# Optimization experiments

Hardware: AMD Instinct MI355X
Metric: run time of the kernel (lower is better)

Reference implementation:

```python
import jax, jax.numpy as jnp
import numpy as np

T, B, IN, H1, H2, OUT = 1024, 512, 20, 128, 64, 3

def _uniform(key, shape, bound):
    return jax.random.uniform(key, shape, jnp.float32, -bound, bound)

def setup_inputs() -> dict:
    key = jax.random.key(0)
    ks = jax.random.split(key, 11)
    b1 = 1.0 / np.sqrt(H1)
    b2 = 1.0 / np.sqrt(H2)
    return {
        "x": jax.random.normal(ks[0], (T, B, IN), jnp.float32),
        "W_ih0": _uniform(ks[1], (4 * H1, IN), b1),
        "W_hh0": _uniform(ks[2], (4 * H1, H1), b1),
        "b_ih0": _uniform(ks[3], (4 * H1,), b1),
        "b_hh0": _uniform(ks[4], (4 * H1,), b1),
        "W_ih1": _uniform(ks[5], (4 * H2, H1), b2),
        "W_hh1": _uniform(ks[6], (4 * H2, H2), b2),
        "b_ih1": _uniform(ks[7], (4 * H2,), b2),
        "b_hh1": _uniform(ks[8], (4 * H2,), b2),
        "W_d": _uniform(ks[9], (OUT, H2), b2),
        "b_d": _uniform(ks[10], (OUT,), b2),
    }

def _lstm_layer(x, W_ih, W_hh, b_ih, b_hh, hidden):
    # x: (T, B, in_dim); PyTorch gate order: i, f, g, o
    batch = x.shape[1]
    x_proj = jnp.einsum("tbi,gi->tbg", x, W_ih) + (b_ih + b_hh)  # (T,B,4H)

    def step(carry, xp):
        h, c = carry
        gates = xp + h @ W_hh.T  # (B,4H)
        i, f, g, o = jnp.split(gates, 4, axis=-1)
        i = jax.nn.sigmoid(i)
        f = jax.nn.sigmoid(f)
        g = jnp.tanh(g)
        o = jax.nn.sigmoid(o)
        c = f * c + i * g
        h = o * jnp.tanh(c)
        return (h, c), h

    h0 = jnp.zeros((batch, hidden), x.dtype)
    c0 = jnp.zeros((batch, hidden), x.dtype)
    _, ys = jax.lax.scan(step, (h0, c0), x_proj)
    return ys  # (T, B, H)

def reference(x, W_ih0, W_hh0, b_ih0, b_hh0, W_ih1, W_hh1, b_ih1, b_hh1, W_d, b_d):
    h1 = _lstm_layer(x, W_ih0, W_hh0, b_ih0, b_hh0, H1)   # (T,B,128)
    h2 = _lstm_layer(h1, W_ih1, W_hh1, b_ih1, b_hh1, H2)  # (T,B,64)
    # Faithful to original: lstm_out[:, -1, :] in seq-first layout picks the
    # last batch element at every timestep -> (T, 64)
    last = h2[:, -1, :]
    act = jax.nn.relu(last)
    # Dropout in eval mode is identity.
    return act @ W_d.T + b_d  # (T, 3)
```

## Files before the change

### kernel.cpp

```cpp
#include <hip/hip_runtime.h>
#include <hip/hip_bf16.h>


#define T_STEPS 1024
#define BATCH   512
#define IN_F    20
#define H1_     128
#define H2_     64
#define OUT_F   3
#define G1_     (4*H1_)
#define G2_     (4*H2_)

typedef float f4 __attribute__((ext_vector_type(4)));
typedef unsigned int u32;
typedef u32 u4 __attribute__((ext_vector_type(4)));
typedef _Float16 h2t __attribute__((ext_vector_type(2)));

__device__ __forceinline__ float sigmoidf_(float x) {
    return 1.0f / (1.0f + __expf(-x));
}
__device__ __forceinline__ float tanhf_(float x) {
    return 1.0f - 2.0f / (__expf(2.0f * x) + 1.0f);
}
__device__ __forceinline__ h2t as_h2(u32 v) {
    union { u32 u; h2t h; } c; c.u = v; return c.h;
}
__device__ __forceinline__ u32 pkh(float a, float b) {
    union { _Float16 h[2]; u32 u; } c;
    c.h[0] = (_Float16)a; c.h[1] = (_Float16)b; return c.u;
}
__device__ __forceinline__ float fdot2_(h2t a, h2t b, float c) {
#if __has_builtin(__builtin_amdgcn_fdot2)
    return __builtin_amdgcn_fdot2(a, b, c, false);
#else
    float d = c;
    asm("v_dot2_f32_f16 %0, %1, %2, %0" : "+v"(d) : "v"(a), "v"(b));
    return d;
#endif
}
__device__ __forceinline__ u4 packq(const float* p) {
    const f4 a = *(const f4*)p;
    const f4 b = *(const f4*)(p + 4);
    u4 pk;
    pk.x = pkh(a.x, a.y); pk.y = pkh(a.z, a.w);
    pk.z = pkh(b.x, b.y); pk.w = pkh(b.z, b.w);
    return pk;
}

#define LO_SCALE_INV 0.000244140625f

#define DOTQ(WQ, HH, HL)                                                      \
    { const u4 hh_ = (HH); const u4 hl_ = (HL);                               \
      a0 = fdot2_(as_h2((WQ).x), as_h2(hh_.x), a0);                           \
      a1 = fdot2_(as_h2((WQ).y), as_h2(hh_.y), a1);                           \
      a0 = fdot2_(as_h2((WQ).z), as_h2(hh_.z), a0);                           \
      a1 = fdot2_(as_h2((WQ).w), as_h2(hh_.w), a1);                           \
      a2 = fdot2_(as_h2((WQ).x), as_h2(hl_.x), a2);                           \
      a3 = fdot2_(as_h2((WQ).y), as_h2(hl_.y), a3);                           \
      a2 = fdot2_(as_h2((WQ).z), as_h2(hl_.z), a2);                           \
      a3 = fdot2_(as_h2((WQ).w), as_h2(hl_.w), a3); }

__global__ void xproj_kernel(const float* __restrict__ x,
                             const float* __restrict__ W_ih0,
                             const float* __restrict__ b_ih0,
                             const float* __restrict__ b_hh0,
                             float* __restrict__ xp1)
{
    const int t = blockIdx.x;
    const int g = threadIdx.x;
    const float* xr = x + ((size_t)t * BATCH + (BATCH - 1)) * IN_F;
    const float* w  = W_ih0 + g * IN_F;
    float acc = b_ih0[g] + b_hh0[g];
#pragma unroll
    for (int i = 0; i < IN_F; ++i) acc = fmaf(xr[i], w[i], acc);
    xp1[t * G1_ + g] = acc;
}

__global__ void pack_kernel(const float* __restrict__ W_hh0,
                            const float* __restrict__ W_hh1,
                            u4* __restrict__ wpk1,
                            u4* __restrict__ wpk2)
{
    const int idx = blockIdx.x * blockDim.x + threadIdx.x;
    if (idx < 8192) {
        const int q = idx >> 10, r = idx & 1023;
        const int g = r & 511, hf = r >> 9;
        wpk1[idx] = packq(W_hh0 + (size_t)g * H1_ + hf * 64 + q * 8);
    } else if (idx < 8192 + 2048) {
        const int i2 = idx - 8192;
        const int q = i2 >> 10, r2 = i2 & 1023;
        const int g2 = r2 & 255, qf = r2 >> 8;
        wpk2[i2] = packq(W_hh1 + (size_t)g2 * H2_ + qf * 16 + q * 8);
    }
}

__global__ __attribute__((amdgpu_flat_work_group_size(1024, 1024),
                          amdgpu_waves_per_eu(4, 4)))
void lstm1_kernel(const float* __restrict__ xp1,
                  const u4* __restrict__ wpk1,
                  float* __restrict__ h1seq)
{
    const int tid = threadIdx.x;
    const int g   = tid & 511;
    const int hf  = tid >> 9;
    const int r   = hf * 512 + g;

    __shared__ u4    shhi[16];
    __shared__ u4    shlo[16];
    __shared__ float sp1[1024];

    if (tid < 16) { shhi[tid] = u4{0,0,0,0}; shlo[tid] = u4{0,0,0,0}; }
    float c1 = 0.0f;
    __syncthreads();

    const u4* wb = wpk1 + r;
    float xp_cur = (hf == 0) ? xp1[g] : 0.0f;

    for (int t = 0; t < T_STEPS; ++t) {
        float xp_next = 0.0f;
        if (hf == 0) {
            const int tn = (t + 1 < T_STEPS) ? (t + 1) : (T_STEPS - 1);
            xp_next = xp1[(size_t)tn * G1_ + g];
        }
        const u4 w0_ = wb[0 * 1024], w1_ = wb[1 * 1024];
        const u4 w2_ = wb[2 * 1024], w3_ = wb[3 * 1024];
        const u4 w4_ = wb[4 * 1024], w5_ = wb[5 * 1024];
        const u4 w6_ = wb[6 * 1024], w7_ = wb[7 * 1024];

        float a0 = 0.f, a1 = 0.f, a2 = 0.f, a3 = 0.f;
        DOTQ(w0_, shhi[hf * 8 + 0], shlo[hf * 8 + 0]);
        DOTQ(w1_, shhi[hf * 8 + 1], shlo[hf * 8 + 1]);
        DOTQ(w2_, shhi[hf * 8 + 2], shlo[hf * 8 + 2]);
        DOTQ(w3_, shhi[hf * 8 + 3], shlo[hf * 8 + 3]);
        DOTQ(w4_, shhi[hf * 8 + 4], shlo[hf * 8 + 4]);
        DOTQ(w5_, shhi[hf * 8 + 5], shlo[hf * 8 + 5]);
        DOTQ(w6_, shhi[hf * 8 + 6], shlo[hf * 8 + 6]);
        DOTQ(w7_, shhi[hf * 8 + 7], shlo[hf * 8 + 7]);

        sp1[g * 2 + hf] = ((a0 + a1) + LO_SCALE_INV * (a2 + a3)) + xp_cur;
        __syncthreads();

        if (tid < H1_) {
            const float vi = sp1[tid * 2]              + sp1[tid * 2 + 1];
            const float vf = sp1[(H1_ + tid) * 2]      + sp1[(H1_ + tid) * 2 + 1];
            const float vg = sp1[(2 * H1_ + tid) * 2]  + sp1[(2 * H1_ + tid) * 2 + 1];
            const float vo = sp1[(3 * H1_ + tid) * 2]  + sp1[(3 * H1_ + tid) * 2 + 1];
            c1 = fmaf(sigmoidf_(vf), c1, sigmoidf_(vi) * tanhf_(vg));
            const float h = sigmoidf_(vo) * tanhf_(c1);
            const _Float16 hh16 = (_Float16)h;
            const float hrem = (h - (float)hh16) * 4096.0f;
            ((_Float16*)shhi)[tid] = hh16;
            ((_Float16*)shlo)[tid] = (_Float16)hrem;
            h1seq[(size_t)t * H1_ + tid] = h;
        }
        __syncthreads();
        xp_cur = xp_next;
    }
}

__global__ void xproj2_kernel(const float* __restrict__ h1seq,
                              const float* __restrict__ W_ih1,
                              const float* __restrict__ b_ih1,
                              const float* __restrict__ b_hh1,
                              float* __restrict__ xp2)
{
    const int t = blockIdx.x;
    const int g = threadIdx.x;
    __shared__ f4 sh[H1_ / 4];
    if (g < H1_ / 4) sh[g] = ((const f4*)(h1seq + (size_t)t * H1_))[g];
    __syncthreads();
    const f4* w = (const f4*)(W_ih1 + (size_t)g * H1_);
    float ax = 0.f, ay = 0.f, az = 0.f, aw = 0.f;
#pragma unroll
    for (int k = 0; k < H1_ / 4; ++k) {
        const f4 h4 = sh[k]; const f4 w4 = w[k];
        ax = fmaf(w4.x, h4.x, ax); ay = fmaf(w4.y, h4.y, ay);
        az = fmaf(w4.z, h4.z, az); aw = fmaf(w4.w, h4.w, aw);
    }
    xp2[(size_t)t * G2_ + g] = ((ax + ay) + (az + aw)) + b_ih1[g] + b_hh1[g];
}

__global__ __attribute__((amdgpu_flat_work_group_size(1024, 1024),
                          amdgpu_waves_per_eu(4, 4)))
void lstm2_kernel(const float* __restrict__ xp2,
                  const u4* __restrict__ wpk2,
                  float* __restrict__ h2seq)
{
    const int tid = threadIdx.x;
    const int g2  = tid & 255;
    const int qf  = tid >> 8;

    __shared__ u4    shhi[8];
    __shared__ u4    shlo[8];
    __shared__ float sp2[1024];

    if (tid < 8) { shhi[tid] = u4{0,0,0,0}; shlo[tid] = u4{0,0,0,0}; }
    float c2 = 0.0f;
    __syncthreads();

    const u4* wb = wpk2 + tid;
    float xp_cur = (qf == 0) ? xp2[g2] : 0.0f;

    for (int t = 0; t < T_STEPS; ++t) {
        float xp_next = 0.0f;
        if (qf == 0) {
            const int tn = (t + 1 < T_STEPS) ? (t + 1) : (T_STEPS - 1);
            xp_next = xp2[(size_t)tn * G2_ + g2];
        }
        const u4 w0_ = wb[0], w1_ = wb[1024];

        float a0 = 0.f, a1 = 0.f, a2 = 0.f, a3 = 0.f;
        DOTQ(w0_, shhi[qf * 2 + 0], shlo[qf * 2 + 0]);
        DOTQ(w1_, shhi[qf * 2 + 1], shlo[qf * 2 + 1]);

        sp2[g2 * 4 + qf] = ((a0 + a1) + LO_SCALE_INV * (a2 + a3)) + xp_cur;
        __syncthreads();

        if (tid < H2_) {
            const f4 pi = ((const f4*)sp2)[tid];
            const f4 pf = ((const f4*)sp2)[H2_ + tid];
            const f4 pg = ((const f4*)sp2)[2 * H2_ + tid];
            const f4 po = ((const f4*)sp2)[3 * H2_ + tid];
            const float vi = (pi.x + pi.y) + (pi.z + pi.w);
            const float vf = (pf.x + pf.y) + (pf.z + pf.w);
            const float vg = (pg.x + pg.y) + (pg.z + pg.w);
            const float vo = (po.x + po.y) + (po.z + po.w);
            c2 = fmaf(sigmoidf_(vf), c2, sigmoidf_(vi) * tanhf_(vg));
            const float h = sigmoidf_(vo) * tanhf_(c2);
            const _Float16 hh16 = (_Float16)h;
            const float hrem = (h - (float)hh16) * 4096.0f;
            ((_Float16*)shhi)[tid] = hh16;
            ((_Float16*)shlo)[tid] = (_Float16)hrem;
            h2seq[(size_t)t * H2_ + tid] = h;
        }
        __syncthreads();
        xp_cur = xp_next;
    }
}

__global__ void head_kernel(const float* __restrict__ h2seq,
                            const float* __restrict__ W_d,
                            const float* __restrict__ b_d,
                            float* __restrict__ out)
{
    const int idx = blockIdx.x * blockDim.x + threadIdx.x;
    if (idx >= T_STEPS * OUT_F) return;
    const int t = idx / OUT_F;
    const int o = idx - t * OUT_F;
    const float* hr = h2seq + (size_t)t * H2_;
    const float* w  = W_d + o * H2_;
    float acc = b_d[o];
#pragma unroll
    for (int j = 0; j < H2_; ++j) acc = fmaf(fmaxf(hr[j], 0.0f), w[j], acc);
    out[idx] = acc;
}

extern "C" void kernel_launch(void* const* d_in, const int* in_sizes, int n_in,
                              void* d_out, int out_size, void* d_ws, size_t ws_size,
                              hipStream_t stream) {
    const float* x     = (const float*)d_in[0];
    const float* W_ih0 = (const float*)d_in[1];
    const float* W_hh0 = (const float*)d_in[2];
    const float* b_ih0 = (const float*)d_in[3];
    const float* b_hh0 = (const float*)d_in[4];
    const float* W_ih1 = (const float*)d_in[5];
    const float* W_hh1 = (const float*)d_in[6];
    const float* b_ih1 = (const float*)d_in[7];
    const float* b_hh1 = (const float*)d_in[8];
    const float* W_d   = (const float*)d_in[9];
    const float* b_d   = (const float*)d_in[10];

    float* out   = (float*)d_out;
    float* xp1   = (float*)d_ws;
    float* h1seq = xp1 + (size_t)T_STEPS * G1_;
    float* h2seq = h1seq + (size_t)T_STEPS * H1_;
    u4*    wpk1  = (u4*)(h2seq + (size_t)T_STEPS * H2_);
    u4*    wpk2  = wpk1 + 8192;
    float* xp2   = xp1;

    hipLaunchKernelGGL(xproj_kernel, dim3(T_STEPS), dim3(G1_), 0, stream,
                       x, W_ih0, b_ih0, b_hh0, xp1);
    hipLaunchKernelGGL(pack_kernel, dim3(40), dim3(256), 0, stream,
                       W_hh0, W_hh1, wpk1, wpk2);
    hipLaunchKernelGGL(lstm1_kernel, dim3(1), dim3(1024), 0, stream,
                       xp1, wpk1, h1seq);
    hipLaunchKernelGGL(xproj2_kernel, dim3(T_STEPS), dim3(G2_), 0, stream,
                       h1seq, W_ih1, b_ih1, b_hh1, xp2);
    hipLaunchKernelGGL(lstm2_kernel, dim3(1), dim3(1024), 0, stream,
                       xp2, wpk2, h2seq);
    hipLaunchKernelGGL(head_kernel, dim3((T_STEPS * OUT_F + 255) / 256), dim3(256),
                       0, stream, h2seq, W_d, b_d, out);
}
```

Before: 1.625 ms.

## Split LSTM1 recurrence into quarter-K slices with two gate rows per thread

Each thread in the layer-1 recurrent kernel now computes two adjacent gate rows over a quarter of the hidden dimension, instead of one gate row over half. The weight packing is reordered to match. Each hidden-state chunk read from shared memory is reused for two rows, which cuts LDS reads per thread. The partial-sum buffer is padded to stride 5 to avoid bank conflicts, and the reduction now sums four partials instead of two.

```diff
diff --git a/kernel.cpp b/kernel.cpp
--- a/kernel.cpp
+++ b/kernel.cpp
@@ -12,6 +12,7 @@
 #define G2_     (4*H2_)
 
 typedef float f4 __attribute__((ext_vector_type(4)));
+typedef float f2 __attribute__((ext_vector_type(2)));
 typedef unsigned int u32;
 typedef u32 u4 __attribute__((ext_vector_type(4)));
 typedef _Float16 h2t __attribute__((ext_vector_type(2)));
@@ -49,16 +50,15 @@
 
 #define LO_SCALE_INV 0.000244140625f
 
-#define DOTQ(WQ, HH, HL)                                                      \
-    { const u4 hh_ = (HH); const u4 hl_ = (HL);                               \
-      a0 = fdot2_(as_h2((WQ).x), as_h2(hh_.x), a0);                           \
-      a1 = fdot2_(as_h2((WQ).y), as_h2(hh_.y), a1);                           \
-      a0 = fdot2_(as_h2((WQ).z), as_h2(hh_.z), a0);                           \
-      a1 = fdot2_(as_h2((WQ).w), as_h2(hh_.w), a1);                           \
-      a2 = fdot2_(as_h2((WQ).x), as_h2(hl_.x), a2);                           \
-      a3 = fdot2_(as_h2((WQ).y), as_h2(hl_.y), a3);                           \
-      a2 = fdot2_(as_h2((WQ).z), as_h2(hl_.z), a2);                           \
-      a3 = fdot2_(as_h2((WQ).w), as_h2(hl_.w), a3); }
+#define DOTQ4(WQ, HH, HL, A0, A1, A2, A3)                                     \
+    { A0 = fdot2_(as_h2((WQ).x), as_h2((HH).x), A0);                          \
+      A1 = fdot2_(as_h2((WQ).y), as_h2((HH).y), A1);                          \
+      A0 = fdot2_(as_h2((WQ).z), as_h2((HH).z), A0);                          \
+      A1 = fdot2_(as_h2((WQ).w), as_h2((HH).w), A1);                          \
+      A2 = fdot2_(as_h2((WQ).x), as_h2((HL).x), A2);                          \
+      A3 = fdot2_(as_h2((WQ).y), as_h2((HL).y), A3);                          \
+      A2 = fdot2_(as_h2((WQ).z), as_h2((HL).z), A2);                          \
+      A3 = fdot2_(as_h2((WQ).w), as_h2((HL).w), A3); }
 
 __global__ void xproj_kernel(const float* __restrict__ x,
                              const float* __restrict__ W_ih0,
@@ -83,14 +83,15 @@
 {
     const int idx = blockIdx.x * blockDim.x + threadIdx.x;
     if (idx < 8192) {
-        const int q = idx >> 10, r = idx & 1023;
-        const int g = r & 511, hf = r >> 9;
-        wpk1[idx] = packq(W_hh0 + (size_t)g * H1_ + hf * 64 + q * 8);
+        const int q = idx >> 10, v = idx & 1023;
+        const int r = v & 255, qf = v >> 8;
+        const int g = 2 * r + (q >> 2);
+        wpk1[idx] = packq(W_hh0 + (size_t)g * H1_ + qf * 32 + (q & 3) * 8);
     } else if (idx < 8192 + 2048) {
         const int i2 = idx - 8192;
-        const int q = i2 >> 10, r2 = i2 & 1023;
-        const int g2 = r2 & 255, qf = r2 >> 8;
-        wpk2[i2] = packq(W_hh1 + (size_t)g2 * H2_ + qf * 16 + q * 8);
+        const int q = i2 >> 10, v2 = i2 & 1023;
+        const int g2 = v2 & 255, qf2 = v2 >> 8;
+        wpk2[i2] = packq(W_hh1 + (size_t)g2 * H2_ + qf2 * 16 + q * 8);
     }
 }
 
@@ -101,57 +102,68 @@
                   float* __restrict__ h1seq)
 {
     const int tid = threadIdx.x;
-    const int g   = tid & 511;
-    const int hf  = tid >> 9;
-    const int r   = hf * 512 + g;
+    const int r   = tid & 255;
+    const int qf  = tid >> 8;
 
     __shared__ u4    shhi[16];
     __shared__ u4    shlo[16];
-    __shared__ float sp1[1024];
+    __shared__ float sp1[G1_ * 5];
 
     if (tid < 16) { shhi[tid] = u4{0,0,0,0}; shlo[tid] = u4{0,0,0,0}; }
     float c1 = 0.0f;
     __syncthreads();
 
-    const u4* wb = wpk1 + r;
-    float xp_cur = (hf == 0) ? xp1[g] : 0.0f;
+    const u4* wb = wpk1 + tid;
+    f2 xp_cur = f2{0.f, 0.f};
+    if (qf == 0) xp_cur = *(const f2*)(xp1 + 2 * r);
 
     for (int t = 0; t < T_STEPS; ++t) {
-        float xp_next = 0.0f;
-        if (hf == 0) {
+        f2 xp_next = f2{0.f, 0.f};
+        if (qf == 0) {
             const int tn = (t + 1 < T_STEPS) ? (t + 1) : (T_STEPS - 1);
-            xp_next = xp1[(size_t)tn * G1_ + g];
+            xp_next = *(const f2*)(xp1 + (size_t)tn * G1_ + 2 * r);
         }
-        const u4 w0_ = wb[0 * 1024], w1_ = wb[1 * 1024];
-        const u4 w2_ = wb[2 * 1024], w3_ = wb[3 * 1024];
-        const u4 w4_ = wb[4 * 1024], w5_ = wb[5 * 1024];
-        const u4 w6_ = wb[6 * 1024], w7_ = wb[7 * 1024];
+        const u4 wa0 = wb[0 * 1024], wa1 = wb[1 * 1024];
+        const u4 wa2 = wb[2 * 1024], wa3 = wb[3 * 1024];
+        const u4 wb0 = wb[4 * 1024], wb1 = wb[5 * 1024];
+        const u4 wb2 = wb[6 * 1024], wb3 = wb[7 * 1024];
+        const u4 hh0 = shhi[qf * 4 + 0], hl0 = shlo[qf * 4 + 0];
+        const u4 hh1 = shhi[qf * 4 + 1], hl1 = shlo[qf * 4 + 1];
+        const u4 hh2 = shhi[qf * 4 + 2], hl2 = shlo[qf * 4 + 2];
+        const u4 hh3 = shhi[qf * 4 + 3], hl3 = shlo[qf * 4 + 3];
 
         float a0 = 0.f, a1 = 0.f, a2 = 0.f, a3 = 0.f;
-        DOTQ(w0_, shhi[hf * 8 + 0], shlo[hf * 8 + 0]);
-        DOTQ(w1_, shhi[hf * 8 + 1], shlo[hf * 8 + 1]);
-        DOTQ(w2_, shhi[hf * 8 + 2], shlo[hf * 8 + 2]);
-        DOTQ(w3_, shhi[hf * 8 + 3], shlo[hf * 8 + 3]);
-        DOTQ(w4_, shhi[hf * 8 + 4], shlo[hf * 8 + 4]);
-        DOTQ(w5_, shhi[hf * 8 + 5], shlo[hf * 8 + 5]);
-        DOTQ(w6_, shhi[hf * 8 + 6], shlo[hf * 8 + 6]);
-        DOTQ(w7_, shhi[hf * 8 + 7], shlo[hf * 8 + 7]);
-
-        sp1[g * 2 + hf] = ((a0 + a1) + LO_SCALE_INV * (a2 + a3)) + xp_cur;
+        float b0 = 0.f, b1 = 0.f, b2 = 0.f, b3 = 0.f;
+        DOTQ4(wa0, hh0, hl0, a0, a1, a2, a3);
+        DOTQ4(wa1, hh1, hl1, a0, a1, a2, a3);
+        DOTQ4(wa2, hh2, hl2, a0, a1, a2, a3);
+        DOTQ4(wa3, hh3, hl3, a0, a1, a2, a3);
+        DOTQ4(wb0, hh0, hl0, b0, b1, b2, b3);
+        DOTQ4(wb1, hh1, hl1, b0, b1, b2, b3);
+        DOTQ4(wb2, hh2, hl2, b0, b1, b2, b3);
+        DOTQ4(wb3, hh3, hl3, b0, b1, b2, b3);
+
+        sp1[(2 * r)     * 5 + qf] = ((a0 + a1) + LO_SCALE_INV * (a2 + a3)) + xp_cur.x;
+        sp1[(2 * r + 1) * 5 + qf] = ((b0 + b1) + LO_SCALE_INV * (b2 + b3)) + xp_cur.y;
         __syncthreads();
 
         if (tid < H1_) {
-            const float vi = sp1[tid * 2]              + sp1[tid * 2 + 1];
-            const float vf = sp1[(H1_ + tid) * 2]      + sp1[(H1_ + tid) * 2 + 1];
-            const float vg = sp1[(2 * H1_ + tid) * 2]  + sp1[(2 * H1_ + tid) * 2 + 1];
-            const float vo = sp1[(3 * H1_ + tid) * 2]  + sp1[(3 * H1_ + tid) * 2 + 1];
+            const int j = tid;
+            const float* s0 = sp1 + j * 5;
+            const float* s1 = sp1 + (H1_ + j) * 5;
+            const float* s2 = sp1 + (2 * H1_ + j) * 5;
+            const float* s3 = sp1 + (3 * H1_ + j) * 5;
+            const float vi = (s0[0] + s0[1]) + (s0[2] + s0[3]);
+            const float vf = (s1[0] + s1[1]) + (s1[2] + s1[3]);
+            const float vg = (s2[0] + s2[1]) + (s2[2] + s2[3]);
+            const float vo = (s3[0] + s3[1]) + (s3[2] + s3[3]);
             c1 = fmaf(sigmoidf_(vf), c1, sigmoidf_(vi) * tanhf_(vg));
             const float h = sigmoidf_(vo) * tanhf_(c1);
             const _Float16 hh16 = (_Float16)h;
             const float hrem = (h - (float)hh16) * 4096.0f;
-            ((_Float16*)shhi)[tid] = hh16;
-            ((_Float16*)shlo)[tid] = (_Float16)hrem;
-            h1seq[(size_t)t * H1_ + tid] = h;
+            ((_Float16*)shhi)[j] = hh16;
+            ((_Float16*)shlo)[j] = (_Float16)hrem;
+            h1seq[(size_t)t * H1_ + j] = h;
         }
         __syncthreads();
         xp_cur = xp_next;
@@ -208,10 +220,12 @@
             xp_next = xp2[(size_t)tn * G2_ + g2];
         }
         const u4 w0_ = wb[0], w1_ = wb[1024];
+        const u4 hh0 = shhi[qf * 2 + 0], hl0 = shlo[qf * 2 + 0];
+        const u4 hh1 = shhi[qf * 2 + 1], hl1 = shlo[qf * 2 + 1];
 
         float a0 = 0.f, a1 = 0.f, a2 = 0.f, a3 = 0.f;
-        DOTQ(w0_, shhi[qf * 2 + 0], shlo[qf * 2 + 0]);
-        DOTQ(w1_, shhi[qf * 2 + 1], shlo[qf * 2 + 1]);
+        DOTQ4(w0_, hh0, hl0, a0, a1, a2, a3);
+        DOTQ4(w1_, hh1, hl1, a0, a1, a2, a3);
 
         sp2[g2 * 4 + qf] = ((a0 + a1) + LO_SCALE_INV * (a2 + a3)) + xp_cur;
         __syncthreads();
```

New measurement: 1.657 ms. About the same (+2.0%).
